# Optimization experiments

Hardware: AMD Instinct MI355X
Metric: run time of the kernel (lower is better)

The kernel has to match this reference:

```python
import jax, jax.numpy as jnp
import numpy as np

ALPHA = 0.929
BETA = 15.99
TAU = 0.0
EPS = 1e-8


def setup_inputs() -> dict:
    key = jax.random.key(0)
    k1, k2 = jax.random.split(key)
    head_outputs = jax.random.normal(k1, (8, 2048, 16, 128), dtype=jnp.float32)
    G = jax.random.normal(k2, (16, 16), dtype=jnp.float32)
    return {"head_outputs": head_outputs, "G": G}


def reference(head_outputs, G):
    B, T, H, d_h = head_outputs.shape
    N = B * T
    outputs = head_outputs.reshape(N, H, d_h)
    mu = outputs.mean(axis=0, keepdims=True)
    # torch .std() is unbiased (ddof=1)
    sigma = outputs.std(axis=0, keepdims=True, ddof=1)
    O_tilde = (outputs - mu) / (sigma + EPS)  # (N, H, d_h)

    # All pairwise cross-correlations in one batched contraction: (H, H, d_h, d_h)
    C = jnp.einsum('nid,nje->ijde', O_tilde, O_tilde) / N
    diff = C - jnp.eye(d_h, dtype=C.dtype)  # subtract_identity=True
    pair_loss = jnp.sum(diff * diff, axis=(2, 3))  # (H, H)

    w = ALPHA + (1.0 - ALPHA) * jax.nn.softplus(-BETA * (G - TAU))  # (H, H)

    upper = jnp.triu(jnp.ones((H, H), dtype=C.dtype), k=1)  # i < j mask
    n_pairs = H * (H - 1) // 2
    loss = jnp.sum(upper * w * pair_loss) / n_pairs
    return loss
```

## Files before the change

kernel.cpp:

```cpp
#include <hip/hip_runtime.h>
#include <hip/hip_bf16.h>

#define N_TOK   16384
#define HDIM    2048
#define NH      16
#define DH      128
#define NPAIRS  120
#define KCHUNKS 8
#define NKT     (N_TOK / 64)
#define KT_PER_CHUNK (NKT / KCHUNKS)
#define PANEL_BYTES 8192

#define SUM_OFF    0u
#define SUMSQ_OFF  8192u
#define MU_OFF     16384u
#define RINV_OFF   24576u
#define PC_OFF     36864u
#define XT_OFF     7901184u

typedef float     f32x4 __attribute__((ext_vector_type(4)));
typedef long long i64t;

#if __has_builtin(__builtin_amdgcn_cvt_pk_fp8_f32)
__device__ __forceinline__ unsigned pk4_fp8(float a, float b, float c, float d) {
    int w = __builtin_amdgcn_cvt_pk_fp8_f32(a, b, 0, false);
    w = __builtin_amdgcn_cvt_pk_fp8_f32(c, d, w, true);
    return (unsigned)w;
}
#else
__device__ __forceinline__ unsigned char f2e4m3_sw(float f) {
    unsigned u = __float_as_uint(f);
    unsigned s = (u >> 24) & 0x80u;
    unsigned a = u & 0x7fffffffu;
    if (a >= 0x43e00000u) return (unsigned char)(s | 0x7eu);
    if (a < 0x3c800000u) {
        float av = __uint_as_float(a);
        int q = (int)rintf(av * 512.0f);
        return (unsigned char)(s | (unsigned)q);
    }
    unsigned lsb = (a >> 20) & 1u;
    a += 0x7ffffu + lsb;
    int e8 = (int)(a >> 23) - 120;
    unsigned m = (a >> 20) & 7u;
    return (unsigned char)(s | ((unsigned)e8 << 3) | m);
}
__device__ __forceinline__ unsigned pk4_fp8(float a, float b, float c, float d) {
    return (unsigned)f2e4m3_sw(a) | ((unsigned)f2e4m3_sw(b) << 8) |
           ((unsigned)f2e4m3_sw(c) << 16) | ((unsigned)f2e4m3_sw(d) << 24);
}
#endif

__global__ __launch_bounds__(256)
void stats_transpose_kernel(const float* __restrict__ X,
                            float* __restrict__ sum, float* __restrict__ sumsq,
                            unsigned char* __restrict__ Xt) {
    __shared__ float tile[64][129];
    __shared__ float sred[4][32][8];
    const int h  = blockIdx.x;
    const int by = blockIdx.y;
    const int n0 = by * 64;
    const int tx = threadIdx.x;
    const int w  = tx >> 6, l = tx & 63;
    const int cq = tx & 31;
    const int rq0 = tx >> 5;

    float4 s  = make_float4(0.f, 0.f, 0.f, 0.f);
    float4 ss = make_float4(0.f, 0.f, 0.f, 0.f);
    #pragma unroll
    for (int it = 0; it < 8; ++it) {
        int r = it * 8 + rq0;
        float4 x = *(const float4*)(X + (size_t)(n0 + r) * HDIM + h * DH + cq * 4);
        s.x += x.x; s.y += x.y; s.z += x.z; s.w += x.w;
        ss.x += x.x * x.x; ss.y += x.y * x.y; ss.z += x.z * x.z; ss.w += x.w * x.w;
        tile[r][cq * 4 + 0] = x.x; tile[r][cq * 4 + 1] = x.y;
        tile[r][cq * 4 + 2] = x.z; tile[r][cq * 4 + 3] = x.w;
    }
    s.x += __shfl_down(s.x, 32);  s.y += __shfl_down(s.y, 32);
    s.z += __shfl_down(s.z, 32);  s.w += __shfl_down(s.w, 32);
    ss.x += __shfl_down(ss.x, 32); ss.y += __shfl_down(ss.y, 32);
    ss.z += __shfl_down(ss.z, 32); ss.w += __shfl_down(ss.w, 32);
    if (l < 32) {
        sred[w][l][0] = s.x;  sred[w][l][1] = s.y;
        sred[w][l][2] = s.z;  sred[w][l][3] = s.w;
        sred[w][l][4] = ss.x; sred[w][l][5] = ss.y;
        sred[w][l][6] = ss.z; sred[w][l][7] = ss.w;
    }
    __syncthreads();
    if (tx < 32) {
        float a0 = 0.f, a1 = 0.f, a2 = 0.f, a3 = 0.f;
        float b0 = 0.f, b1 = 0.f, b2 = 0.f, b3 = 0.f;
        #pragma unroll
        for (int w2 = 0; w2 < 4; ++w2) {
            a0 += sred[w2][tx][0]; a1 += sred[w2][tx][1];
            a2 += sred[w2][tx][2]; a3 += sred[w2][tx][3];
            b0 += sred[w2][tx][4]; b1 += sred[w2][tx][5];
            b2 += sred[w2][tx][6]; b3 += sred[w2][tx][7];
        }
        int c = h * DH + tx * 4;
        atomicAdd(&sum[c + 0], a0);  atomicAdd(&sum[c + 1], a1);
        atomicAdd(&sum[c + 2], a2);  atomicAdd(&sum[c + 3], a3);
        atomicAdd(&sumsq[c + 0], b0); atomicAdd(&sumsq[c + 1], b1);
        atomicAdd(&sumsq[c + 2], b2); atomicAdd(&sumsq[c + 3], b3);
    }
    unsigned char* panel = Xt + ((size_t)h * NKT + by) * PANEL_BYTES;
    #pragma unroll
    for (int it = 0; it < 2; ++it) {
        int q = it * 256 + tx;
        int c = q >> 2, o = q & 3;
        uint4 pk;
        pk.x = pk4_fp8(tile[o*16+ 0][c], tile[o*16+ 1][c], tile[o*16+ 2][c], tile[o*16+ 3][c]);
        pk.y = pk4_fp8(tile[o*16+ 4][c], tile[o*16+ 5][c], tile[o*16+ 6][c], tile[o*16+ 7][c]);
        pk.z = pk4_fp8(tile[o*16+ 8][c], tile[o*16+ 9][c], tile[o*16+10][c], tile[o*16+11][c]);
        pk.w = pk4_fp8(tile[o*16+12][c], tile[o*16+13][c], tile[o*16+14][c], tile[o*16+15][c]);
        *(uint4*)(panel + c * 64 + o * 16) = pk;
    }
}

__global__ void finalize_kernel(const float* __restrict__ sum, const float* __restrict__ sumsq,
                                float* __restrict__ mu, float* __restrict__ rinv) {
    int c = blockIdx.x * 256 + threadIdx.x;
    float m = sum[c] * (1.f / (float)N_TOK);
    float var = (sumsq[c] - (float)N_TOK * m * m) * (1.f / (float)(N_TOK - 1));
    var = fmaxf(var, 0.f);
    mu[c]   = m;
    rinv[c] = 1.f / (sqrtf(var) + 1e-8f);
}

__device__ __forceinline__ void gload16(const void* gsrc, void* ldst) {
    __builtin_amdgcn_global_load_lds(
        (const __attribute__((address_space(1))) unsigned int*)gsrc,
        (__attribute__((address_space(3))) unsigned int*)ldst,
        16, 0, 0);
}

__global__ __launch_bounds__(256, 4)
void gram_kernel(const unsigned char* __restrict__ Xt, float* __restrict__ pairC) {
    const int kc = blockIdx.x;
    const int p  = blockIdx.y;
    int i = 0, rem = p;
    while (rem >= NH - 1 - i) { rem -= NH - 1 - i; ++i; }
    const int j = i + 1 + rem;

    __shared__ alignas(16) unsigned char ldsA[PANEL_BYTES];
    __shared__ alignas(16) unsigned char ldsB[PANEL_BYTES];

    const int tx = threadIdx.x;
    const int w  = tx >> 6, l = tx & 63;
    const int wm = w >> 1, wn = w & 1;
    const int l15 = l & 15, quad = l >> 4;

    unsigned int goff[2];
    int ldsOff[2];
    #pragma unroll
    for (int s = 0; s < 2; ++s) {
        int cfl = s * 256 + tx;
        int r = cfl >> 2, cl = cfl & 3;
        int cc = cl ^ ((r >> 1) & 3);
        goff[s]   = (unsigned int)(r * 64 + cc * 16);
        ldsOff[s] = s * 4096 + w * 1024;
    }
    const char* Abase = (const char*)Xt + ((size_t)i * NKT + (size_t)kc * KT_PER_CHUNK) * PANEL_BYTES;
    const char* Bbase = (const char*)Xt + ((size_t)j * NKT + (size_t)kc * KT_PER_CHUNK) * PANEL_BYTES;

    f32x4 acc[4][4];
    #pragma unroll
    for (int mi = 0; mi < 4; ++mi)
        #pragma unroll
        for (int ni = 0; ni < 4; ++ni)
            acc[mi][ni] = (f32x4){0.f, 0.f, 0.f, 0.f};

    const int usw = l15 & 6;
    for (int kt = 0; kt < KT_PER_CHUNK; ++kt) {
        const char* pa = Abase + (size_t)kt * PANEL_BYTES;
        const char* pb = Bbase + (size_t)kt * PANEL_BYTES;
        gload16(pa + goff[0], (char*)ldsA + ldsOff[0]);
        gload16(pa + goff[1], (char*)ldsA + ldsOff[1]);
        gload16(pb + goff[0], (char*)ldsB + ldsOff[0]);
        gload16(pb + goff[1], (char*)ldsB + ldsOff[1]);
        __syncthreads();

        #pragma unroll
        for (int kh = 0; kh < 2; ++kh) {
            const int u = (kh * 4 + quad) ^ usw;
            i64t a[4], b[4];
            #pragma unroll
            for (int mi = 0; mi < 4; ++mi) {
                int r = wm * 64 + mi * 16 + l15;
                a[mi] = *(const i64t*)(ldsA + r * 64 + u * 8);
            }
            #pragma unroll
            for (int ni = 0; ni < 4; ++ni) {
                int r = wn * 64 + ni * 16 + l15;
                b[ni] = *(const i64t*)(ldsB + r * 64 + u * 8);
            }
            #pragma unroll
            for (int mi = 0; mi < 4; ++mi)
                #pragma unroll
                for (int ni = 0; ni < 4; ++ni)
                    acc[mi][ni] = __builtin_amdgcn_mfma_f32_16x16x32_fp8_fp8(
                        a[mi], b[ni], acc[mi][ni], 0, 0, 0);
        }
        __syncthreads();
    }

    float* pc = pairC + (size_t)p * (DH * DH);
    #pragma unroll
    for (int mi = 0; mi < 4; ++mi)
        #pragma unroll
        for (int ni = 0; ni < 4; ++ni)
            #pragma unroll
            for (int r = 0; r < 4; ++r) {
                int row = wm * 64 + mi * 16 + quad * 4 + r;
                int col = wn * 64 + ni * 16 + l15;
                atomicAdd(&pc[row * DH + col], acc[mi][ni][r]);
            }
}

__global__ void pair_reduce_kernel(const float* __restrict__ pairC, const float* __restrict__ G,
                                   const float* __restrict__ mu, const float* __restrict__ rinv,
                                   float* __restrict__ out) {
    int p = blockIdx.x;
    int i = 0, rem = p;
    while (rem >= NH - 1 - i) { rem -= NH - 1 - i; ++i; }
    int j = i + 1 + rem;
    __shared__ float smui[DH], smuj[DH], sri[DH], srj[DH];
    if (threadIdx.x < DH) {
        smui[threadIdx.x] = mu[i * DH + threadIdx.x];
        smuj[threadIdx.x] = mu[j * DH + threadIdx.x];
        sri[threadIdx.x]  = rinv[i * DH + threadIdx.x];
        srj[threadIdx.x]  = rinv[j * DH + threadIdx.x];
    }
    __syncthreads();
    const float invN = 1.f / (float)N_TOK;
    const float* pc = pairC + (size_t)p * (DH * DH);
    float s = 0.f;
    for (int idx = threadIdx.x; idx < DH * DH; idx += 256) {
        int d = idx >> 7, e = idx & 127;
        float cn = (pc[idx] * invN - smui[d] * smuj[e]) * sri[d] * srj[e];
        float diff = cn - ((d == e) ? 1.f : 0.f);
        s += diff * diff;
    }
    for (int o = 32; o; o >>= 1) s += __shfl_down(s, o);
    __shared__ float red[4];
    if ((threadIdx.x & 63) == 0) red[threadIdx.x >> 6] = s;
    __syncthreads();
    if (threadIdx.x == 0) {
        float t = red[0] + red[1] + red[2] + red[3];
        float x = -15.99f * (G[i * NH + j] - 0.0f);
        float sp = (x > 20.f) ? x : log1pf(expf(x));
        float wgt = 0.929f + (1.f - 0.929f) * sp;
        atomicAdd(out, wgt * t * (1.f / (float)NPAIRS));
    }
}

extern "C" void kernel_launch(void* const* d_in, const int* in_sizes, int n_in,
                              void* d_out, int out_size, void* d_ws, size_t ws_size,
                              hipStream_t stream) {
    const float* X = (const float*)d_in[0];
    const float* G = (const float*)d_in[1];
    float* out = (float*)d_out;
    char* ws = (char*)d_ws;

    float*         sum   = (float*)(ws + SUM_OFF);
    float*         sumsq = (float*)(ws + SUMSQ_OFF);
    float*         mu    = (float*)(ws + MU_OFF);
    float*         rinv  = (float*)(ws + RINV_OFF);
    float*         pairC = (float*)(ws + PC_OFF);
    unsigned char* Xt    = (unsigned char*)(ws + XT_OFF);

    hipMemsetAsync(ws + SUM_OFF, 0, 16384, stream);
    hipMemsetAsync(ws + PC_OFF, 0, (size_t)NPAIRS * DH * DH * 4, stream);
    hipMemsetAsync(d_out, 0, 4, stream);

    stats_transpose_kernel<<<dim3(16, 256), 256, 0, stream>>>(X, sum, sumsq, Xt);
    finalize_kernel<<<8, 256, 0, stream>>>(sum, sumsq, mu, rinv);
    gram_kernel<<<dim3(KCHUNKS, NPAIRS), 256, 0, stream>>>(Xt, pairC);
    pair_reduce_kernel<<<NPAIRS, 256, 0, stream>>>(pairC, G, mu, rinv, out);
}
```

Baseline: 297.0 us.

## Double-buffer gram LDS panels, widen fragment loads, fold finalize into reduce

The gram kernel now uses two LDS buffers per operand and prefetches the next k-tile while computing the current one, so each iteration needs one barrier instead of two. The panel byte layout is changed so each lane reads its two fp8 k-fragments with a single 16-byte LDS load. The separate finalize kernel is removed: mean and inverse std are recomputed inside pair_reduce, and the two workspace memsets are merged into one. This doubles LDS per block, which may lower occupancy, and relies on the new transpose layout matching the new swizzled reads.

```diff
diff --git a/kernel.cpp b/kernel.cpp
--- a/kernel.cpp
+++ b/kernel.cpp
@@ -13,13 +13,12 @@
 
 #define SUM_OFF    0u
 #define SUMSQ_OFF  8192u
-#define MU_OFF     16384u
-#define RINV_OFF   24576u
-#define PC_OFF     36864u
-#define XT_OFF     7901184u
+#define PC_OFF     16384u
+#define XT_OFF     7880704u
 
 typedef float     f32x4 __attribute__((ext_vector_type(4)));
 typedef long long i64t;
+typedef long long i64x2 __attribute__((ext_vector_type(2)));
 
 #if __has_builtin(__builtin_amdgcn_cvt_pk_fp8_f32)
 __device__ __forceinline__ unsigned pk4_fp8(float a, float b, float c, float d) {
@@ -106,24 +105,15 @@
     #pragma unroll
     for (int it = 0; it < 2; ++it) {
         int q = it * 256 + tx;
-        int c = q >> 2, o = q & 3;
+        int d = q >> 2, c = q & 3;
+        int t0 = c * 8;
         uint4 pk;
-        pk.x = pk4_fp8(tile[o*16+ 0][c], tile[o*16+ 1][c], tile[o*16+ 2][c], tile[o*16+ 3][c]);
-        pk.y = pk4_fp8(tile[o*16+ 4][c], tile[o*16+ 5][c], tile[o*16+ 6][c], tile[o*16+ 7][c]);
-        pk.z = pk4_fp8(tile[o*16+ 8][c], tile[o*16+ 9][c], tile[o*16+10][c], tile[o*16+11][c]);
-        pk.w = pk4_fp8(tile[o*16+12][c], tile[o*16+13][c], tile[o*16+14][c], tile[o*16+15][c]);
-        *(uint4*)(panel + c * 64 + o * 16) = pk;
-    }
-}
-
-__global__ void finalize_kernel(const float* __restrict__ sum, const float* __restrict__ sumsq,
-                                float* __restrict__ mu, float* __restrict__ rinv) {
-    int c = blockIdx.x * 256 + threadIdx.x;
-    float m = sum[c] * (1.f / (float)N_TOK);
-    float var = (sumsq[c] - (float)N_TOK * m * m) * (1.f / (float)(N_TOK - 1));
-    var = fmaxf(var, 0.f);
-    mu[c]   = m;
-    rinv[c] = 1.f / (sqrtf(var) + 1e-8f);
+        pk.x = pk4_fp8(tile[t0+ 0][d], tile[t0+ 1][d], tile[t0+ 2][d], tile[t0+ 3][d]);
+        pk.y = pk4_fp8(tile[t0+ 4][d], tile[t0+ 5][d], tile[t0+ 6][d], tile[t0+ 7][d]);
+        pk.z = pk4_fp8(tile[32+t0+0][d], tile[32+t0+1][d], tile[32+t0+2][d], tile[32+t0+3][d]);
+        pk.w = pk4_fp8(tile[32+t0+4][d], tile[32+t0+5][d], tile[32+t0+6][d], tile[32+t0+7][d]);
+        *(uint4*)(panel + d * 64 + c * 16) = pk;
+    }
 }
 
 __device__ __forceinline__ void gload16(const void* gsrc, void* ldst) {
@@ -141,8 +131,8 @@
     while (rem >= NH - 1 - i) { rem -= NH - 1 - i; ++i; }
     const int j = i + 1 + rem;
 
-    __shared__ alignas(16) unsigned char ldsA[PANEL_BYTES];
-    __shared__ alignas(16) unsigned char ldsB[PANEL_BYTES];
+    __shared__ alignas(16) unsigned char ldsA[2][PANEL_BYTES];
+    __shared__ alignas(16) unsigned char ldsB[2][PANEL_BYTES];
 
     const int tx = threadIdx.x;
     const int w  = tx >> 6, l = tx & 63;
@@ -153,10 +143,10 @@
     int ldsOff[2];
     #pragma unroll
     for (int s = 0; s < 2; ++s) {
-        int cfl = s * 256 + tx;
-        int r = cfl >> 2, cl = cfl & 3;
-        int cc = cl ^ ((r >> 1) & 3);
-        goff[s]   = (unsigned int)(r * 64 + cc * 16);
+        int pi = s * 256 + tx;
+        int r = pi >> 2, cp = pi & 3;
+        int c = cp ^ ((r >> 1) & 3);
+        goff[s]   = (unsigned int)(r * 64 + c * 16);
         ldsOff[s] = s * 4096 + w * 1024;
     }
     const char* Abase = (const char*)Xt + ((size_t)i * NKT + (size_t)kc * KT_PER_CHUNK) * PANEL_BYTES;
@@ -169,38 +159,48 @@
         for (int ni = 0; ni < 4; ++ni)
             acc[mi][ni] = (f32x4){0.f, 0.f, 0.f, 0.f};
 
-    const int usw = l15 & 6;
+    const int rsw = (l15 >> 1) & 3;
+    const int cp  = quad ^ rsw;
+
+    {
+        const char* pa = Abase;
+        const char* pb = Bbase;
+        gload16(pa + goff[0], (char*)ldsA[0] + ldsOff[0]);
+        gload16(pa + goff[1], (char*)ldsA[0] + ldsOff[1]);
+        gload16(pb + goff[0], (char*)ldsB[0] + ldsOff[0]);
+        gload16(pb + goff[1], (char*)ldsB[0] + ldsOff[1]);
+    }
+
     for (int kt = 0; kt < KT_PER_CHUNK; ++kt) {
-        const char* pa = Abase + (size_t)kt * PANEL_BYTES;
-        const char* pb = Bbase + (size_t)kt * PANEL_BYTES;
-        gload16(pa + goff[0], (char*)ldsA + ldsOff[0]);
-        gload16(pa + goff[1], (char*)ldsA + ldsOff[1]);
-        gload16(pb + goff[0], (char*)ldsB + ldsOff[0]);
-        gload16(pb + goff[1], (char*)ldsB + ldsOff[1]);
+        const int cur = kt & 1;
         __syncthreads();
-
-        #pragma unroll
-        for (int kh = 0; kh < 2; ++kh) {
-            const int u = (kh * 4 + quad) ^ usw;
-            i64t a[4], b[4];
-            #pragma unroll
-            for (int mi = 0; mi < 4; ++mi) {
-                int r = wm * 64 + mi * 16 + l15;
-                a[mi] = *(const i64t*)(ldsA + r * 64 + u * 8);
-            }
-            #pragma unroll
-            for (int ni = 0; ni < 4; ++ni) {
-                int r = wn * 64 + ni * 16 + l15;
-                b[ni] = *(const i64t*)(ldsB + r * 64 + u * 8);
-            }
+        if (kt + 1 < KT_PER_CHUNK) {
+            const char* pa = Abase + (size_t)(kt + 1) * PANEL_BYTES;
+            const char* pb = Bbase + (size_t)(kt + 1) * PANEL_BYTES;
+            gload16(pa + goff[0], (char*)ldsA[1 - cur] + ldsOff[0]);
+            gload16(pa + goff[1], (char*)ldsA[1 - cur] + ldsOff[1]);
+            gload16(pb + goff[0], (char*)ldsB[1 - cur] + ldsOff[0]);
+            gload16(pb + goff[1], (char*)ldsB[1 - cur] + ldsOff[1]);
+        }
+        i64x2 a[4], b[4];
+        #pragma unroll
+        for (int mi = 0; mi < 4; ++mi) {
+            int r = wm * 64 + mi * 16 + l15;
+            a[mi] = *(const i64x2*)(ldsA[cur] + r * 64 + cp * 16);
+        }
+        #pragma unroll
+        for (int ni = 0; ni < 4; ++ni) {
+            int r = wn * 64 + ni * 16 + l15;
+            b[ni] = *(const i64x2*)(ldsB[cur] + r * 64 + cp * 16);
+        }
+        #pragma unroll
+        for (int kh = 0; kh < 2; ++kh)
             #pragma unroll
             for (int mi = 0; mi < 4; ++mi)
                 #pragma unroll
                 for (int ni = 0; ni < 4; ++ni)
                     acc[mi][ni] = __builtin_amdgcn_mfma_f32_16x16x32_fp8_fp8(
-                        a[mi], b[ni], acc[mi][ni], 0, 0, 0);
-        }
-        __syncthreads();
+                        a[mi][kh], b[ni][kh], acc[mi][ni], 0, 0, 0);
     }
 
     float* pc = pairC + (size_t)p * (DH * DH);
@@ -217,18 +217,23 @@
 }
 
 __global__ void pair_reduce_kernel(const float* __restrict__ pairC, const float* __restrict__ G,
-                                   const float* __restrict__ mu, const float* __restrict__ rinv,
+                                   const float* __restrict__ sum, const float* __restrict__ sumsq,
                                    float* __restrict__ out) {
     int p = blockIdx.x;
     int i = 0, rem = p;
     while (rem >= NH - 1 - i) { rem -= NH - 1 - i; ++i; }
     int j = i + 1 + rem;
     __shared__ float smui[DH], smuj[DH], sri[DH], srj[DH];
-    if (threadIdx.x < DH) {
-        smui[threadIdx.x] = mu[i * DH + threadIdx.x];
-        smuj[threadIdx.x] = mu[j * DH + threadIdx.x];
-        sri[threadIdx.x]  = rinv[i * DH + threadIdx.x];
-        srj[threadIdx.x]  = rinv[j * DH + threadIdx.x];
+    {
+        int t = threadIdx.x & 127;
+        int h = (threadIdx.x < 128) ? i : j;
+        int c = h * DH + t;
+        float m = sum[c] * (1.f / (float)N_TOK);
+        float var = (sumsq[c] - (float)N_TOK * m * m) * (1.f / (float)(N_TOK - 1));
+        var = fmaxf(var, 0.f);
+        float rv = 1.f / (sqrtf(var) + 1e-8f);
+        if (threadIdx.x < 128) { smui[t] = m; sri[t] = rv; }
+        else                   { smuj[t] = m; srj[t] = rv; }
     }
     __syncthreads();
     const float invN = 1.f / (float)N_TOK;
@@ -263,17 +268,13 @@
 
     float*         sum   = (float*)(ws + SUM_OFF);
     float*         sumsq = (float*)(ws + SUMSQ_OFF);
-    float*         mu    = (float*)(ws + MU_OFF);
-    float*         rinv  = (float*)(ws + RINV_OFF);
     float*         pairC = (float*)(ws + PC_OFF);
     unsigned char* Xt    = (unsigned char*)(ws + XT_OFF);
 
-    hipMemsetAsync(ws + SUM_OFF, 0, 16384, stream);
-    hipMemsetAsync(ws + PC_OFF, 0, (size_t)NPAIRS * DH * DH * 4, stream);
+    hipMemsetAsync(ws, 0, PC_OFF + (size_t)NPAIRS * DH * DH * 4, stream);
     hipMemsetAsync(d_out, 0, 4, stream);
 
     stats_transpose_kernel<<<dim3(16, 256), 256, 0, stream>>>(X, sum, sumsq, Xt);
-    finalize_kernel<<<8, 256, 0, stream>>>(sum, sumsq, mu, rinv);
     gram_kernel<<<dim3(KCHUNKS, NPAIRS), 256, 0, stream>>>(Xt, pairC);
-    pair_reduce_kernel<<<NPAIRS, 256, 0, stream>>>(pairC, G, mu, rinv, out);
-}
+    pair_reduce_kernel<<<NPAIRS, 256, 0, stream>>>(pairC, G, sum, sumsq, out);
+}
```

Measured after the change: 300.3 us. Within noise of the previous version (+1.1%).

## Switch gram to 32x32x64 scaled FP8 MFMA and replace stats atomics with partials

Applied to the files above, without the earlier changes.

The gram kernel now uses the MI355 mfma_scale 32x32x64 f8f6f4 instruction with unit scales. It loads two k-panels per phase with 128-bit LDS reads, which halves the sync count and cuts atomic epilogue traffic per output element. The stats kernel writes per-block partial sums to a workspace instead of doing global atomics, and finalize reduces them serially over 256 blocks. This removes atomic contention but adds a serial loop in the small finalize kernel and larger LDS use, which could lower occupancy.

```diff
diff --git a/kernel.cpp b/kernel.cpp
--- a/kernel.cpp
+++ b/kernel.cpp
@@ -9,50 +9,28 @@
 #define KCHUNKS 8
 #define NKT     (N_TOK / 64)
 #define KT_PER_CHUNK (NKT / KCHUNKS)
+#define NPHASE  (KT_PER_CHUNK / 2)
 #define PANEL_BYTES 8192
 
-#define SUM_OFF    0u
-#define SUMSQ_OFF  8192u
-#define MU_OFF     16384u
-#define RINV_OFF   24576u
-#define PC_OFF     36864u
-#define XT_OFF     7901184u
-
-typedef float     f32x4 __attribute__((ext_vector_type(4)));
-typedef long long i64t;
-
-#if __has_builtin(__builtin_amdgcn_cvt_pk_fp8_f32)
+#define MU_OFF     0u
+#define RINV_OFF   8192u
+#define PC_OFF     16384u
+#define PSUM_OFF   7880704u
+#define PSQ_OFF    9977856u
+#define XT_OFF     12075008u
+
+typedef int   i32x8  __attribute__((ext_vector_type(8)));
+typedef float f32x16 __attribute__((ext_vector_type(16)));
+
 __device__ __forceinline__ unsigned pk4_fp8(float a, float b, float c, float d) {
     int w = __builtin_amdgcn_cvt_pk_fp8_f32(a, b, 0, false);
     w = __builtin_amdgcn_cvt_pk_fp8_f32(c, d, w, true);
     return (unsigned)w;
 }
-#else
-__device__ __forceinline__ unsigned char f2e4m3_sw(float f) {
-    unsigned u = __float_as_uint(f);
-    unsigned s = (u >> 24) & 0x80u;
-    unsigned a = u & 0x7fffffffu;
-    if (a >= 0x43e00000u) return (unsigned char)(s | 0x7eu);
-    if (a < 0x3c800000u) {
-        float av = __uint_as_float(a);
-        int q = (int)rintf(av * 512.0f);
-        return (unsigned char)(s | (unsigned)q);
-    }
-    unsigned lsb = (a >> 20) & 1u;
-    a += 0x7ffffu + lsb;
-    int e8 = (int)(a >> 23) - 120;
-    unsigned m = (a >> 20) & 7u;
-    return (unsigned char)(s | ((unsigned)e8 << 3) | m);
-}
-__device__ __forceinline__ unsigned pk4_fp8(float a, float b, float c, float d) {
-    return (unsigned)f2e4m3_sw(a) | ((unsigned)f2e4m3_sw(b) << 8) |
-           ((unsigned)f2e4m3_sw(c) << 16) | ((unsigned)f2e4m3_sw(d) << 24);
-}
-#endif
 
 __global__ __launch_bounds__(256)
 void stats_transpose_kernel(const float* __restrict__ X,
-                            float* __restrict__ sum, float* __restrict__ sumsq,
+                            float* __restrict__ psum, float* __restrict__ psq,
                             unsigned char* __restrict__ Xt) {
     __shared__ float tile[64][129];
     __shared__ float sred[4][32][8];
@@ -96,31 +74,35 @@
             b0 += sred[w2][tx][4]; b1 += sred[w2][tx][5];
             b2 += sred[w2][tx][6]; b3 += sred[w2][tx][7];
         }
-        int c = h * DH + tx * 4;
-        atomicAdd(&sum[c + 0], a0);  atomicAdd(&sum[c + 1], a1);
-        atomicAdd(&sum[c + 2], a2);  atomicAdd(&sum[c + 3], a3);
-        atomicAdd(&sumsq[c + 0], b0); atomicAdd(&sumsq[c + 1], b1);
-        atomicAdd(&sumsq[c + 2], b2); atomicAdd(&sumsq[c + 3], b3);
+        size_t o = (size_t)by * HDIM + h * DH + tx * 4;
+        *(float4*)(psum + o) = make_float4(a0, a1, a2, a3);
+        *(float4*)(psq  + o) = make_float4(b0, b1, b2, b3);
     }
     unsigned char* panel = Xt + ((size_t)h * NKT + by) * PANEL_BYTES;
     #pragma unroll
     for (int it = 0; it < 2; ++it) {
         int q = it * 256 + tx;
-        int c = q >> 2, o = q & 3;
+        int d = q >> 2, c = q & 3;
+        int t0 = c * 16;
         uint4 pk;
-        pk.x = pk4_fp8(tile[o*16+ 0][c], tile[o*16+ 1][c], tile[o*16+ 2][c], tile[o*16+ 3][c]);
-        pk.y = pk4_fp8(tile[o*16+ 4][c], tile[o*16+ 5][c], tile[o*16+ 6][c], tile[o*16+ 7][c]);
-        pk.z = pk4_fp8(tile[o*16+ 8][c], tile[o*16+ 9][c], tile[o*16+10][c], tile[o*16+11][c]);
-        pk.w = pk4_fp8(tile[o*16+12][c], tile[o*16+13][c], tile[o*16+14][c], tile[o*16+15][c]);
-        *(uint4*)(panel + c * 64 + o * 16) = pk;
-    }
-}
-
-__global__ void finalize_kernel(const float* __restrict__ sum, const float* __restrict__ sumsq,
+        pk.x = pk4_fp8(tile[t0+ 0][d], tile[t0+ 1][d], tile[t0+ 2][d], tile[t0+ 3][d]);
+        pk.y = pk4_fp8(tile[t0+ 4][d], tile[t0+ 5][d], tile[t0+ 6][d], tile[t0+ 7][d]);
+        pk.z = pk4_fp8(tile[t0+ 8][d], tile[t0+ 9][d], tile[t0+10][d], tile[t0+11][d]);
+        pk.w = pk4_fp8(tile[t0+12][d], tile[t0+13][d], tile[t0+14][d], tile[t0+15][d]);
+        *(uint4*)(panel + d * 64 + c * 16) = pk;
+    }
+}
+
+__global__ void finalize_kernel(const float* __restrict__ psum, const float* __restrict__ psq,
                                 float* __restrict__ mu, float* __restrict__ rinv) {
     int c = blockIdx.x * 256 + threadIdx.x;
-    float m = sum[c] * (1.f / (float)N_TOK);
-    float var = (sumsq[c] - (float)N_TOK * m * m) * (1.f / (float)(N_TOK - 1));
+    float s = 0.f, q = 0.f;
+    for (int by = 0; by < 256; ++by) {
+        s += psum[(size_t)by * HDIM + c];
+        q += psq[(size_t)by * HDIM + c];
+    }
+    float m = s * (1.f / (float)N_TOK);
+    float var = (q - (float)N_TOK * m * m) * (1.f / (float)(N_TOK - 1));
     var = fmaxf(var, 0.f);
     mu[c]   = m;
     rinv[c] = 1.f / (sqrtf(var) + 1e-8f);
@@ -141,78 +123,95 @@
     while (rem >= NH - 1 - i) { rem -= NH - 1 - i; ++i; }
     const int j = i + 1 + rem;
 
-    __shared__ alignas(16) unsigned char ldsA[PANEL_BYTES];
-    __shared__ alignas(16) unsigned char ldsB[PANEL_BYTES];
+    __shared__ alignas(16) unsigned char ldsA[2 * PANEL_BYTES];
+    __shared__ alignas(16) unsigned char ldsB[2 * PANEL_BYTES];
 
     const int tx = threadIdx.x;
     const int w  = tx >> 6, l = tx & 63;
     const int wm = w >> 1, wn = w & 1;
-    const int l15 = l & 15, quad = l >> 4;
-
-    unsigned int goff[2];
-    int ldsOff[2];
-    #pragma unroll
-    for (int s = 0; s < 2; ++s) {
+    const int l31 = l & 31, h = l >> 5;
+
+    unsigned int goff[4];
+    int ldsOff[4];
+    #pragma unroll
+    for (int s = 0; s < 4; ++s) {
         int cfl = s * 256 + tx;
-        int r = cfl >> 2, cl = cfl & 3;
-        int cc = cl ^ ((r >> 1) & 3);
-        goff[s]   = (unsigned int)(r * 64 + cc * 16);
+        int pnl = cfl >> 9, q = cfl & 511;
+        int r = q >> 2, cp = q & 3;
+        int csrc = cp ^ ((r >> 1) & 3);
+        goff[s]   = (unsigned int)(pnl * PANEL_BYTES + r * 64 + csrc * 16);
         ldsOff[s] = s * 4096 + w * 1024;
     }
     const char* Abase = (const char*)Xt + ((size_t)i * NKT + (size_t)kc * KT_PER_CHUNK) * PANEL_BYTES;
     const char* Bbase = (const char*)Xt + ((size_t)j * NKT + (size_t)kc * KT_PER_CHUNK) * PANEL_BYTES;
 
-    f32x4 acc[4][4];
-    #pragma unroll
-    for (int mi = 0; mi < 4; ++mi)
-        #pragma unroll
-        for (int ni = 0; ni < 4; ++ni)
-            acc[mi][ni] = (f32x4){0.f, 0.f, 0.f, 0.f};
-
-    const int usw = l15 & 6;
-    for (int kt = 0; kt < KT_PER_CHUNK; ++kt) {
-        const char* pa = Abase + (size_t)kt * PANEL_BYTES;
-        const char* pb = Bbase + (size_t)kt * PANEL_BYTES;
-        gload16(pa + goff[0], (char*)ldsA + ldsOff[0]);
-        gload16(pa + goff[1], (char*)ldsA + ldsOff[1]);
-        gload16(pb + goff[0], (char*)ldsB + ldsOff[0]);
-        gload16(pb + goff[1], (char*)ldsB + ldsOff[1]);
+    f32x16 acc[2][2];
+    #pragma unroll
+    for (int mi = 0; mi < 2; ++mi)
+        #pragma unroll
+        for (int ni = 0; ni < 2; ++ni)
+            #pragma unroll
+            for (int q = 0; q < 16; ++q)
+                acc[mi][ni][q] = 0.f;
+
+    const int G = (l31 >> 1) & 3;
+    const int cp0 = (2 * h) ^ G;
+    const int cp1 = cp0 ^ 1;
+
+    for (int ph = 0; ph < NPHASE; ++ph) {
+        const char* pa = Abase + (size_t)ph * (2 * PANEL_BYTES);
+        const char* pb = Bbase + (size_t)ph * (2 * PANEL_BYTES);
+        #pragma unroll
+        for (int s = 0; s < 4; ++s)
+            gload16(pa + goff[s], (char*)ldsA + ldsOff[s]);
+        #pragma unroll
+        for (int s = 0; s < 4; ++s)
+            gload16(pb + goff[s], (char*)ldsB + ldsOff[s]);
         __syncthreads();
 
         #pragma unroll
-        for (int kh = 0; kh < 2; ++kh) {
-            const int u = (kh * 4 + quad) ^ usw;
-            i64t a[4], b[4];
-            #pragma unroll
-            for (int mi = 0; mi < 4; ++mi) {
-                int r = wm * 64 + mi * 16 + l15;
-                a[mi] = *(const i64t*)(ldsA + r * 64 + u * 8);
+        for (int sub = 0; sub < 2; ++sub) {
+            const int pbase = sub * PANEL_BYTES;
+            i32x8 a[2], b[2];
+            #pragma unroll
+            for (int mi = 0; mi < 2; ++mi) {
+                int r = wm * 64 + mi * 32 + l31;
+                uint4 lo = *(const uint4*)(ldsA + pbase + r * 64 + cp0 * 16);
+                uint4 hi = *(const uint4*)(ldsA + pbase + r * 64 + cp1 * 16);
+                a[mi] = (i32x8){(int)lo.x,(int)lo.y,(int)lo.z,(int)lo.w,
+                                (int)hi.x,(int)hi.y,(int)hi.z,(int)hi.w};
             }
             #pragma unroll
-            for (int ni = 0; ni < 4; ++ni) {
-                int r = wn * 64 + ni * 16 + l15;
-                b[ni] = *(const i64t*)(ldsB + r * 64 + u * 8);
+            for (int ni = 0; ni < 2; ++ni) {
+                int r = wn * 64 + ni * 32 + l31;
+                uint4 lo = *(const uint4*)(ldsB + pbase + r * 64 + cp0 * 16);
+                uint4 hi = *(const uint4*)(ldsB + pbase + r * 64 + cp1 * 16);
+                b[ni] = (i32x8){(int)lo.x,(int)lo.y,(int)lo.z,(int)lo.w,
+                                (int)hi.x,(int)hi.y,(int)hi.z,(int)hi.w};
             }
             #pragma unroll
-            for (int mi = 0; mi < 4; ++mi)
+            for (int mi = 0; mi < 2; ++mi)
                 #pragma unroll
-                for (int ni = 0; ni < 4; ++ni)
-                    acc[mi][ni] = __builtin_amdgcn_mfma_f32_16x16x32_fp8_fp8(
-                        a[mi], b[ni], acc[mi][ni], 0, 0, 0);
+                for (int ni = 0; ni < 2; ++ni)
+                    acc[mi][ni] = __builtin_amdgcn_mfma_scale_f32_32x32x64_f8f6f4(
+                        a[mi], b[ni], acc[mi][ni],
+                        0, 0,
+                        0, 127,
+                        0, 127);
         }
         __syncthreads();
     }
 
     float* pc = pairC + (size_t)p * (DH * DH);
     #pragma unroll
-    for (int mi = 0; mi < 4; ++mi)
-        #pragma unroll
-        for (int ni = 0; ni < 4; ++ni)
-            #pragma unroll
-            for (int r = 0; r < 4; ++r) {
-                int row = wm * 64 + mi * 16 + quad * 4 + r;
-                int col = wn * 64 + ni * 16 + l15;
-                atomicAdd(&pc[row * DH + col], acc[mi][ni][r]);
+    for (int mi = 0; mi < 2; ++mi)
+        #pragma unroll
+        for (int ni = 0; ni < 2; ++ni)
+            #pragma unroll
+            for (int q = 0; q < 16; ++q) {
+                int row = wm * 64 + mi * 32 + (q & 3) + 8 * (q >> 2) + 4 * h;
+                int col = wn * 64 + ni * 32 + l31;
+                atomicAdd(&pc[row * DH + col], acc[mi][ni][q]);
             }
 }
 
@@ -261,19 +260,18 @@
     float* out = (float*)d_out;
     char* ws = (char*)d_ws;
 
-    float*         sum   = (float*)(ws + SUM_OFF);
-    float*         sumsq = (float*)(ws + SUMSQ_OFF);
     float*         mu    = (float*)(ws + MU_OFF);
     float*         rinv  = (float*)(ws + RINV_OFF);
     float*         pairC = (float*)(ws + PC_OFF);
+    float*         psum  = (float*)(ws + PSUM_OFF);
+    float*         psq   = (float*)(ws + PSQ_OFF);
     unsigned char* Xt    = (unsigned char*)(ws + XT_OFF);
 
-    hipMemsetAsync(ws + SUM_OFF, 0, 16384, stream);
     hipMemsetAsync(ws + PC_OFF, 0, (size_t)NPAIRS * DH * DH * 4, stream);
     hipMemsetAsync(d_out, 0, 4, stream);
 
-    stats_transpose_kernel<<<dim3(16, 256), 256, 0, stream>>>(X, sum, sumsq, Xt);
-    finalize_kernel<<<8, 256, 0, stream>>>(sum, sumsq, mu, rinv);
+    stats_transpose_kernel<<<dim3(16, 256), 256, 0, stream>>>(X, psum, psq, Xt);
+    finalize_kernel<<<8, 256, 0, stream>>>(psum, psq, mu, rinv);
     gram_kernel<<<dim3(KCHUNKS, NPAIRS), 256, 0, stream>>>(Xt, pairC);
     pair_reduce_kernel<<<NPAIRS, 256, 0, stream>>>(pairC, G, mu, rinv, out);
 }
```

Result: slower. 312.7 us (+5.3%).
